# Optimization experiments

Measured on AMD Instinct MI355X. Metric: run time of the kernel, lower is better.

## Reference

```python
import jax, jax.numpy as jnp
import numpy as np

N0, N1, N2 = 30000, 90000, 60000          # nodes, edges, triangles
D_IN, D_OUT, HEADS = 256, 128, 4
NNZ0, NNZ1, NNZ2 = 960000, 180000, 180000  # sparse incidence nnz


def setup_inputs() -> dict:
    key = jax.random.key(0)
    ks = jax.random.split(key, 18)
    s = 0.05
    return {
        "x0": jax.random.normal(ks[0], (N0, D_IN), dtype=jnp.float32),
        "x1": jax.random.normal(ks[1], (N1, D_IN), dtype=jnp.float32),
        "x2": jax.random.normal(ks[2], (N2, D_IN), dtype=jnp.float32),
        "rows0": jax.random.randint(ks[3], (NNZ0,), 0, N0),
        "cols0": jax.random.randint(ks[4], (NNZ0,), 0, N0),
        "rows1": jax.random.randint(ks[5], (NNZ1,), 0, N0),
        "cols1": jax.random.randint(ks[6], (NNZ1,), 0, N1),
        "rows2": jax.random.randint(ks[7], (NNZ2,), 0, N0),
        "cols2": jax.random.randint(ks[8], (NNZ2,), 0, N2),
        # per-head parameters (SATLayer_regular), stacked on leading head axis
        "W1": jax.random.normal(ks[9], (HEADS, D_IN, D_OUT), dtype=jnp.float32) * s,
        "b1": jax.random.normal(ks[10], (HEADS, D_OUT), dtype=jnp.float32) * s,
        "a1_w": jax.random.normal(ks[11], (HEADS, D_OUT), dtype=jnp.float32) * s,
        "a1_b": jax.random.normal(ks[12], (HEADS,), dtype=jnp.float32) * s,
        "a2_w": jax.random.normal(ks[13], (HEADS, D_OUT), dtype=jnp.float32) * s,
        "a2_b": jax.random.normal(ks[14], (HEADS,), dtype=jnp.float32) * s,
        "Wagg": jax.random.normal(ks[15], (HEADS, 4 * D_OUT, D_OUT), dtype=jnp.float32) * s,
        "bagg": jax.random.normal(ks[16], (HEADS, D_OUT), dtype=jnp.float32) * s,
    }


def reference(x0, x1, x2, rows0, cols0, rows1, cols1, rows2, cols2,
              W1, b1, a1_w, a1_b, a2_w, a2_b, Wagg, bagg):
    n0 = x0.shape[0]

    def sat_head(W1h, b1h, a1wh, a1bh, a2wh, a2bh, Waggh, baggh):
        # shared Linearlayer1 + ReLU applied to all simplex levels
        xi0 = jax.nn.relu(x0 @ W1h + b1h)   # [n0, d]
        xj1 = jax.nn.relu(x1 @ W1h + b1h)   # [n1, d]
        xj2 = jax.nn.relu(x2 @ W1h + b1h)   # [n2, d]
        a1 = xi0 @ a1wh + a1bh              # [n0] attention source term

        def attention_agg(xj, rows, cols):
            a2 = xj @ a2wh + a2bh                              # [nj]
            att = jax.nn.sigmoid(a1[rows] + a2[cols])          # [nnz]
            msg = att[:, None] * xj[cols]                      # [nnz, d]
            return jax.ops.segment_sum(msg, rows, num_segments=n0)

        agg0 = attention_agg(xi0, rows0, cols0)
        agg1 = attention_agg(xj1, rows1, cols1)
        agg2 = attention_agg(xj2, rows2, cols2)
        cat = jnp.concatenate([xi0, agg0, agg1, agg2], axis=1)  # [n0, 4d]
        return cat @ Waggh + baggh                              # [n0, d]

    # stack over heads, then mean (layer0_1 + torch.mean)
    outs = jax.vmap(sat_head)(W1, b1, a1_w, a1_b, a2_w, a2_b, Wagg, bagg)
    return jnp.mean(outs, axis=0)
```

## Files before the change

### kernel.cpp

```cpp
#include <hip/hip_runtime.h>

typedef __attribute__((ext_vector_type(8))) short short8;
typedef __attribute__((ext_vector_type(4))) float f32x4;
typedef unsigned short ushort_t;
typedef unsigned int uint32;

#define N0 30000
#define N1 90000
#define N2 60000
#define P0 30208
#define P1 90112
#define P2 60032
#define S1OFF 30208
#define S2OFF 120320
#define MPAD 180352
#define MT_ALL 1409
#define MT0 236
#define MT1 704
#define MT2 469
#define NNZ_ALL 1320000

__device__ __forceinline__ float bf2f(ushort_t u) {
    union { uint32 i; float f; } v; v.i = ((uint32)u) << 16; return v.f;
}
__device__ __forceinline__ ushort_t f2bf(float f) {
    union { float f; uint32 i; } v; v.f = f;
    uint32 x = v.i;
    x += ((x >> 16) & 1u) + 0x7FFFu;
    return (ushort_t)(x >> 16);
}

__global__ __launch_bounds__(256) void prep_w(const float* __restrict__ W1,
                                              const float* __restrict__ Wagg,
                                              const float* __restrict__ bagg,
                                              ushort_t* __restrict__ W1t,
                                              ushort_t* __restrict__ Wgt,
                                              ushort_t* __restrict__ WgtC,
                                              float* __restrict__ bsum) {
    int idx = blockIdx.x * blockDim.x + threadIdx.x;
    if (idx < 131072) {
        int h = idx >> 15, rem = idx & 32767, n = rem >> 8, k = rem & 255;
        W1t[idx] = f2bf(W1[((size_t)h * 256 + k) * 128 + n]);
    }
    if (idx < 196608) {
        int h = idx / 49152, rem = idx % 49152;
        int l = rem / 16384, rem2 = rem % 16384, n = rem2 >> 7, k = rem2 & 127;
        Wgt[idx] = f2bf(Wagg[((size_t)h * 512 + (l + 1) * 128 + k) * 128 + n]);
    }
    if (idx < 65536) {
        int n = idx >> 9, kk = idx & 511, h = kk >> 7, k = kk & 127;
        WgtC[idx] = f2bf(Wagg[((size_t)h * 512 + k) * 128 + n]);
    }
    if (idx < 128) {
        float s = 0.f;
        #pragma unroll
        for (int h = 0; h < 4; ++h) s += bagg[h * 128 + idx];
        bsum[idx] = s;
    }
}

__global__ __launch_bounds__(256) void csr_zero(int* __restrict__ cur) {
    int i = blockIdx.x * blockDim.x + threadIdx.x;
    if (i < P0) cur[i] = 0;
}

__global__ __launch_bounds__(256) void csr_hist(const int* __restrict__ rows, int nE,
                                                int* __restrict__ cur) {
    int i = blockIdx.x * blockDim.x + threadIdx.x;
    if (i < nE) atomicAdd(cur + rows[i], 1);
}

__global__ __launch_bounds__(1024) void csr_scan(int* __restrict__ cur,
                                                 int* __restrict__ rowPtr) {
    __shared__ int ssum[1024];
    const int t = threadIdx.x;
    const int base = t * 30;
    int loc[30];
    int s = 0;
    #pragma unroll
    for (int i = 0; i < 30; ++i) {
        int r = base + i;
        int v = (r < N0) ? cur[r] : 0;
        loc[i] = s; s += v;
    }
    ssum[t] = s;
    __syncthreads();
    for (int off = 1; off < 1024; off <<= 1) {
        int v = (t >= off) ? ssum[t - off] : 0;
        __syncthreads();
        ssum[t] += v;
        __syncthreads();
    }
    int carry = (t == 0) ? 0 : ssum[t - 1];
    #pragma unroll
    for (int i = 0; i < 30; ++i) {
        int r = base + i;
        if (r < N0) {
            int p = carry + loc[i];
            rowPtr[r] = p;
            cur[r] = p;
        }
    }
    if (t == 0) rowPtr[N0] = NNZ_ALL;
}

__global__ __launch_bounds__(256) void csr_scatter(const int* __restrict__ rows,
                                                   const int* __restrict__ cols,
                                                   int nE, int Sl,
                                                   int* __restrict__ cur,
                                                   int* __restrict__ sortedCg) {
    int i = blockIdx.x * blockDim.x + threadIdx.x;
    if (i < nE) {
        int pos = atomicAdd(cur + rows[i], 1);
        sortedCg[pos] = Sl + cols[i];
    }
}

__global__ __launch_bounds__(256) void gemm_x(const float* __restrict__ x0,
                                              const float* __restrict__ x1,
                                              const float* __restrict__ x2,
                                              const ushort_t* __restrict__ W1t,
                                              const float* __restrict__ b1,
                                              ushort_t* __restrict__ Y) {
    __shared__ ushort_t As[128 * 264];
    __shared__ ushort_t Bs[128 * 40];
    const int tid = threadIdx.x;
    const int lane = tid & 63;
    const int wid = tid >> 6;
    const int wm = wid >> 1, wn = wid & 1;
    const int l15 = lane & 15, lg = lane >> 4;
    const int r0 = blockIdx.x * 128;

    const float* src; int jbase, nreal;
    if (r0 < P0)          { src = x0; jbase = r0;         nreal = N0; }
    else if (r0 < S2OFF)  { src = x1; jbase = r0 - S1OFF; nreal = N1; }
    else                  { src = x2; jbase = r0 - S2OFF; nreal = N2; }

    for (int c = 0; c < 32; ++c) {
        int f = tid + c * 256;
        int row = f >> 6, col4 = f & 63;
        int j = jbase + row;
        float vx = 0.f, vy = 0.f, vz = 0.f, vw = 0.f;
        if (j < nreal) {
            const float4 v = *(const float4*)(src + (size_t)j * 256 + col4 * 4);
            vx = v.x; vy = v.y; vz = v.z; vw = v.w;
        }
        ushort_t o[4] __attribute__((aligned(8)));
        o[0] = f2bf(vx); o[1] = f2bf(vy); o[2] = f2bf(vz); o[3] = f2bf(vw);
        *(uint2*)(As + row * 264 + col4 * 4) = *(const uint2*)o;
    }
    __syncthreads();

    for (int h = 0; h < 4; ++h) {
        f32x4 acc[4][4] = {};
        const ushort_t* Bh = W1t + h * 32768;
        for (int kt = 0; kt < 256; kt += 32) {
            #pragma unroll
            for (int u = 0; u < 2; ++u) {
                int g = tid * 2 + u;
                int n = g >> 2, kc = g & 3;
                *(uint4*)(Bs + n * 40 + kc * 8) = *(const uint4*)(Bh + n * 256 + kt + kc * 8);
            }
            __syncthreads();
            short8 af[4], bfr[4];
            #pragma unroll
            for (int m = 0; m < 4; ++m)
                af[m] = *(const short8*)(As + (wm * 64 + m * 16 + l15) * 264 + kt + lg * 8);
            #pragma unroll
            for (int n = 0; n < 4; ++n)
                bfr[n] = *(const short8*)(Bs + (wn * 64 + n * 16 + l15) * 40 + lg * 8);
            #pragma unroll
            for (int m = 0; m < 4; ++m)
                #pragma unroll
                for (int n = 0; n < 4; ++n)
                    acc[m][n] = __builtin_amdgcn_mfma_f32_16x16x32_bf16(af[m], bfr[n], acc[m][n], 0, 0, 0);
            __syncthreads();
        }
        #pragma unroll
        for (int n = 0; n < 4; ++n) {
            int col = wn * 64 + n * 16 + l15;
            float bb = b1[h * 128 + col];
            #pragma unroll
            for (int m = 0; m < 4; ++m)
            #pragma unroll
            for (int j = 0; j < 4; ++j) {
                int row = r0 + wm * 64 + m * 16 + lg * 4 + j;
                float v = acc[m][n][j] + bb;
                v = v > 0.f ? v : 0.f;
                Y[(size_t)row * 512 + h * 128 + col] = f2bf(v);
            }
        }
    }
}

template<int EPI>
__global__ __launch_bounds__(256)
void gemm_k(const ushort_t* A, int ldA, int strideA,
            const ushort_t* __restrict__ B, int K, int strideB,
            ushort_t* outBF, int outLd, int strideOut,
            float* __restrict__ outF,
            const float* __restrict__ bias, int strideBias,
            int rowGuard)
{
    __shared__ ushort_t As[128 * 40];
    __shared__ ushort_t Bs[128 * 40];
    const int tid = threadIdx.x;
    const int lane = tid & 63;
    const int wid = tid >> 6;
    const int wm = wid >> 1, wn = wid & 1;
    const int r0 = blockIdx.x * 128;
    const int l15 = lane & 15, lg = lane >> 4;

    A += (size_t)blockIdx.y * strideA;
    B += (size_t)blockIdx.y * strideB;
    if (outBF) outBF += (size_t)blockIdx.y * strideOut;
    if (bias) bias += (size_t)blockIdx.y * strideBias;

    f32x4 acc[4][4] = {};

    for (int kt = 0; kt < K; kt += 32) {
        #pragma unroll
        for (int c = 0; c < 2; ++c) {
            int idx = tid + c * 256;
            int row = idx >> 2, kc = idx & 3;
            uint4 va = *(const uint4*)(A + (size_t)(r0 + row) * ldA + kt + kc * 8);
            *(uint4*)(As + row * 40 + kc * 8) = va;
            uint4 vb = *(const uint4*)(B + (size_t)row * K + kt + kc * 8);
            *(uint4*)(Bs + row * 40 + kc * 8) = vb;
        }
        __syncthreads();
        short8 af[4], bfr[4];
        #pragma unroll
        for (int m = 0; m < 4; ++m)
            af[m] = *(const short8*)(As + (wm * 64 + m * 16 + l15) * 40 + lg * 8);
        #pragma unroll
        for (int n = 0; n < 4; ++n)
            bfr[n] = *(const short8*)(Bs + (wn * 64 + n * 16 + l15) * 40 + lg * 8);
        #pragma unroll
        for (int m = 0; m < 4; ++m)
            #pragma unroll
            for (int n = 0; n < 4; ++n)
                acc[m][n] = __builtin_amdgcn_mfma_f32_16x16x32_bf16(af[m], bfr[n], acc[m][n], 0, 0, 0);
        __syncthreads();
    }

    #pragma unroll
    for (int m = 0; m < 4; ++m)
    #pragma unroll
    for (int n = 0; n < 4; ++n)
    #pragma unroll
    for (int j = 0; j < 4; ++j) {
        int row = r0 + wm * 64 + m * 16 + lg * 4 + j;
        int col = wn * 64 + n * 16 + l15;
        float v = acc[m][n][j];
        if (EPI == 1) {
            outBF[(size_t)row * outLd + col] = f2bf(v);
        } else {
            if (row < rowGuard) outF[(size_t)row * 128 + col] = 0.25f * (v + bias[col]);
        }
    }
}

__global__ __launch_bounds__(256) void attn_coef(const ushort_t* __restrict__ Y,
                                                 const float* __restrict__ a1w,
                                                 const float* __restrict__ a1b,
                                                 const float* __restrict__ a2w,
                                                 const float* __restrict__ a2b,
                                                 float* __restrict__ a1o,
                                                 float* __restrict__ a2o) {
    int tid = threadIdx.x, lane = tid & 63, wid = tid >> 6;
    int R = blockIdx.x * 4 + wid;
    int h = lane >> 4, s = lane & 15;
    uint4 v = *(const uint4*)(Y + (size_t)R * 512 + h * 128 + s * 8);
    const ushort_t* u = (const ushort_t*)&v;
    float x[8];
    #pragma unroll
    for (int i = 0; i < 8; ++i) x[i] = bf2f(u[i]);
    float d2 = 0.f;
    #pragma unroll
    for (int i = 0; i < 8; ++i) d2 += x[i] * a2w[h * 128 + s * 8 + i];
    #pragma unroll
    for (int off = 1; off < 16; off <<= 1) d2 += __shfl_xor(d2, off);
    if (s == 0) a2o[(size_t)h * MPAD + R] = d2 + a2b[h];
    if (R < N0) {
        float d1 = 0.f;
        #pragma unroll
        for (int i = 0; i < 8; ++i) d1 += x[i] * a1w[h * 128 + s * 8 + i];
        #pragma unroll
        for (int off = 1; off < 16; off <<= 1) d1 += __shfl_xor(d1, off);
        if (s == 0) a1o[(size_t)h * P0 + R] = d1 + a1b[h];
    }
}

__global__ __launch_bounds__(256) void pull_agg(const int* __restrict__ rowPtr,
                                                const int* __restrict__ sortedCg,
                                                const float* __restrict__ a1,
                                                const float* __restrict__ a2,
                                                const ushort_t* __restrict__ z,
                                                float* __restrict__ out) {
    int w = blockIdx.x * 4 + (threadIdx.x >> 6);
    if (w >= N0) return;
    const int lane = threadIdx.x & 63;
    const int h = lane >> 4, g = lane & 15;

    const float a1r = a1[(size_t)h * P0 + w];
    const float* a2h = a2 + (size_t)h * MPAD;
    int beg = rowPtr[w], end = rowPtr[w + 1];

    float acc[8] = {0.f, 0.f, 0.f, 0.f, 0.f, 0.f, 0.f, 0.f};
    for (int e = beg; e < end; ++e) {
        int cg = sortedCg[e];
        float s = a1r + a2h[cg];
        float att = 0.25f / (1.f + __expf(-s));
        uint4 v = *(const uint4*)(z + (size_t)cg * 512 + lane * 8);
        const ushort_t* u = (const ushort_t*)&v;
        #pragma unroll
        for (int j = 0; j < 8; ++j) acc[j] += att * bf2f(u[j]);
    }
    #pragma unroll
    for (int j = 0; j < 8; ++j) {
        acc[j] += __shfl_xor(acc[j], 16);
        acc[j] += __shfl_xor(acc[j], 32);
    }
    float2* p = (float2*)(out + (size_t)w * 128 + g * 8 + h * 2);
    float2 o = *p;
    o.x += acc[h * 2 + 0];
    o.y += acc[h * 2 + 1];
    *p = o;
}

extern "C" void kernel_launch(void* const* d_in, const int* in_sizes, int n_in,
                              void* d_out, int out_size, void* d_ws, size_t ws_size,
                              hipStream_t stream) {
    const float* x0   = (const float*)d_in[0];
    const float* x1   = (const float*)d_in[1];
    const float* x2   = (const float*)d_in[2];
    const int* rows0  = (const int*)d_in[3];
    const int* cols0  = (const int*)d_in[4];
    const int* rows1  = (const int*)d_in[5];
    const int* cols1  = (const int*)d_in[6];
    const int* rows2  = (const int*)d_in[7];
    const int* cols2  = (const int*)d_in[8];
    const float* W1   = (const float*)d_in[9];
    const float* b1   = (const float*)d_in[10];
    const float* a1w  = (const float*)d_in[11];
    const float* a1b  = (const float*)d_in[12];
    const float* a2w  = (const float*)d_in[13];
    const float* a2b  = (const float*)d_in[14];
    const float* Wagg = (const float*)d_in[15];
    const float* bagg = (const float*)d_in[16];
    float* out = (float*)d_out;
    char* ws = (char*)d_ws;

    ushort_t* Y      = (ushort_t*)(ws);
    float*    a1o    = (float*)(ws + 184680448);
    float*    a2o    = (float*)(ws + 185163776);
    ushort_t* W1t    = (ushort_t*)(ws + 188049408);
    ushort_t* Wgt    = (ushort_t*)(ws + 188311552);
    ushort_t* WgtC   = (ushort_t*)(ws + 188704768);
    float*    bsum   = (float*)(ws + 188835840);
    int*      cur    = (int*)(ws + 188836352);
    int*      rowPtr = (int*)(ws + 188957184);
    int*      srtCg  = (int*)(ws + 189078016);

    csr_zero<<<(P0 + 255) / 256, 256, 0, stream>>>(cur);
    csr_hist<<<(960000 + 255) / 256, 256, 0, stream>>>(rows0, 960000, cur);
    csr_hist<<<(180000 + 255) / 256, 256, 0, stream>>>(rows1, 180000, cur);
    csr_hist<<<(180000 + 255) / 256, 256, 0, stream>>>(rows2, 180000, cur);
    csr_scan<<<1, 1024, 0, stream>>>(cur, rowPtr);
    csr_scatter<<<(960000 + 255) / 256, 256, 0, stream>>>(rows0, cols0, 960000, 0, cur, srtCg);
    csr_scatter<<<(180000 + 255) / 256, 256, 0, stream>>>(rows1, cols1, 180000, S1OFF, cur, srtCg);
    csr_scatter<<<(180000 + 255) / 256, 256, 0, stream>>>(rows2, cols2, 180000, S2OFF, cur, srtCg);

    prep_w<<<768, 256, 0, stream>>>(W1, Wagg, bagg, W1t, Wgt, WgtC, bsum);
    gemm_x<<<MT_ALL, 256, 0, stream>>>(x0, x1, x2, W1t, b1, Y);

    attn_coef<<<MPAD / 4, 256, 0, stream>>>(Y, a1w, a1b, a2w, a2b, a1o, a2o);

    gemm_k<2><<<dim3(MT0, 1), 256, 0, stream>>>(
        Y, 512, 0, WgtC, 512, 0, nullptr, 0, 0, out, bsum, 0, N0);

    gemm_k<1><<<dim3(MT0, 4), 256, 0, stream>>>(
        Y, 512, 128, Wgt + 0 * 16384, 128, 3 * 16384, Y, 512, 128, nullptr, nullptr, 0, 0);
    gemm_k<1><<<dim3(MT1, 4), 256, 0, stream>>>(
        Y + (size_t)S1OFF * 512, 512, 128, Wgt + 1 * 16384, 128, 3 * 16384,
        Y + (size_t)S1OFF * 512, 512, 128, nullptr, nullptr, 0, 0);
    gemm_k<1><<<dim3(MT2, 4), 256, 0, stream>>>(
        Y + (size_t)S2OFF * 512, 512, 128, Wgt + 2 * 16384, 128, 3 * 16384,
        Y + (size_t)S2OFF * 512, 512, 128, nullptr, nullptr, 0, 0);

    pull_agg<<<(N0 + 3) / 4, 256, 0, stream>>>(rowPtr, srtCg, a1o, a2o, Y, out);
}
```

Baseline: 699.3 us.

## Fuse attention coefficients into per-level Z GEMM and split CSR per level

Folds the attention-coefficient dot products into a single merged GEMM that projects each head's activations by the level-specific aggregation weights. The full 128x128 tile and K=128 are staged in LDS once, removing the separate attn_coef pass and its extra read of Y. The CSR build is split into three per-level structures with three pull_agg launches, and the pull loop is unrolled by two edges. The three launches add traffic on the output accumulator, and the fused kernel uses far more shared memory per block, which may reduce occupancy.

Measured after the change: 645.1 us. -7.7%, faster.

```diff
diff --git a/kernel.cpp b/kernel.cpp
--- a/kernel.cpp
+++ b/kernel.cpp
@@ -9,16 +9,15 @@
 #define N1 90000
 #define N2 60000
 #define P0 30208
-#define P1 90112
-#define P2 60032
 #define S1OFF 30208
 #define S2OFF 120320
 #define MPAD 180352
 #define MT_ALL 1409
 #define MT0 236
-#define MT1 704
-#define MT2 469
-#define NNZ_ALL 1320000
+#define NE0 960000
+#define NE1 180000
+#define NE2 180000
+#define CSTRIDE 30720
 
 __device__ __forceinline__ float bf2f(ushort_t u) {
     union { uint32 i; float f; } v; v.i = ((uint32)u) << 16; return v.f;
@@ -61,7 +60,7 @@
 
 __global__ __launch_bounds__(256) void csr_zero(int* __restrict__ cur) {
     int i = blockIdx.x * blockDim.x + threadIdx.x;
-    if (i < P0) cur[i] = 0;
+    if (i < 3 * CSTRIDE) cur[i] = 0;
 }
 
 __global__ __launch_bounds__(256) void csr_hist(const int* __restrict__ rows, int nE,
@@ -70,9 +69,14 @@
     if (i < nE) atomicAdd(cur + rows[i], 1);
 }
 
-__global__ __launch_bounds__(1024) void csr_scan(int* __restrict__ cur,
-                                                 int* __restrict__ rowPtr) {
+__global__ __launch_bounds__(1024) void csr_scan(int* __restrict__ curA,
+                                                 int* __restrict__ rowPtrA,
+                                                 int nE0, int nE1, int nE2) {
     __shared__ int ssum[1024];
+    const int b = blockIdx.x;
+    int* cur = curA + b * CSTRIDE;
+    int* rowPtr = rowPtrA + b * CSTRIDE;
+    const int nE = (b == 0) ? nE0 : (b == 1 ? nE1 : nE2);
     const int t = threadIdx.x;
     const int base = t * 30;
     int loc[30];
@@ -101,7 +105,7 @@
             cur[r] = p;
         }
     }
-    if (t == 0) rowPtr[N0] = NNZ_ALL;
+    if (t == 0) rowPtr[N0] = nE;
 }
 
 __global__ __launch_bounds__(256) void csr_scatter(const int* __restrict__ rows,
@@ -193,14 +197,11 @@
     }
 }
 
-template<int EPI>
 __global__ __launch_bounds__(256)
-void gemm_k(const ushort_t* A, int ldA, int strideA,
-            const ushort_t* __restrict__ B, int K, int strideB,
-            ushort_t* outBF, int outLd, int strideOut,
-            float* __restrict__ outF,
-            const float* __restrict__ bias, int strideBias,
-            int rowGuard)
+void gemm_init(const ushort_t* __restrict__ A,
+               const ushort_t* __restrict__ B,
+               float* __restrict__ outF,
+               const float* __restrict__ bias)
 {
     __shared__ ushort_t As[128 * 40];
     __shared__ ushort_t Bs[128 * 40];
@@ -211,21 +212,16 @@
     const int r0 = blockIdx.x * 128;
     const int l15 = lane & 15, lg = lane >> 4;
 
-    A += (size_t)blockIdx.y * strideA;
-    B += (size_t)blockIdx.y * strideB;
-    if (outBF) outBF += (size_t)blockIdx.y * strideOut;
-    if (bias) bias += (size_t)blockIdx.y * strideBias;
-
     f32x4 acc[4][4] = {};
 
-    for (int kt = 0; kt < K; kt += 32) {
+    for (int kt = 0; kt < 512; kt += 32) {
         #pragma unroll
         for (int c = 0; c < 2; ++c) {
             int idx = tid + c * 256;
             int row = idx >> 2, kc = idx & 3;
-            uint4 va = *(const uint4*)(A + (size_t)(r0 + row) * ldA + kt + kc * 8);
+            uint4 va = *(const uint4*)(A + (size_t)(r0 + row) * 512 + kt + kc * 8);
             *(uint4*)(As + row * 40 + kc * 8) = va;
-            uint4 vb = *(const uint4*)(B + (size_t)row * K + kt + kc * 8);
+            uint4 vb = *(const uint4*)(B + (size_t)row * 512 + kt + kc * 8);
             *(uint4*)(Bs + row * 40 + kc * 8) = vb;
         }
         __syncthreads();
@@ -252,43 +248,95 @@
     for (int j = 0; j < 4; ++j) {
         int row = r0 + wm * 64 + m * 16 + lg * 4 + j;
         int col = wn * 64 + n * 16 + l15;
-        float v = acc[m][n][j];
-        if (EPI == 1) {
-            outBF[(size_t)row * outLd + col] = f2bf(v);
-        } else {
-            if (row < rowGuard) outF[(size_t)row * 128 + col] = 0.25f * (v + bias[col]);
-        }
-    }
-}
-
-__global__ __launch_bounds__(256) void attn_coef(const ushort_t* __restrict__ Y,
-                                                 const float* __restrict__ a1w,
-                                                 const float* __restrict__ a1b,
-                                                 const float* __restrict__ a2w,
-                                                 const float* __restrict__ a2b,
-                                                 float* __restrict__ a1o,
-                                                 float* __restrict__ a2o) {
-    int tid = threadIdx.x, lane = tid & 63, wid = tid >> 6;
-    int R = blockIdx.x * 4 + wid;
-    int h = lane >> 4, s = lane & 15;
-    uint4 v = *(const uint4*)(Y + (size_t)R * 512 + h * 128 + s * 8);
-    const ushort_t* u = (const ushort_t*)&v;
-    float x[8];
-    #pragma unroll
-    for (int i = 0; i < 8; ++i) x[i] = bf2f(u[i]);
-    float d2 = 0.f;
-    #pragma unroll
-    for (int i = 0; i < 8; ++i) d2 += x[i] * a2w[h * 128 + s * 8 + i];
-    #pragma unroll
-    for (int off = 1; off < 16; off <<= 1) d2 += __shfl_xor(d2, off);
-    if (s == 0) a2o[(size_t)h * MPAD + R] = d2 + a2b[h];
-    if (R < N0) {
-        float d1 = 0.f;
-        #pragma unroll
-        for (int i = 0; i < 8; ++i) d1 += x[i] * a1w[h * 128 + s * 8 + i];
-        #pragma unroll
-        for (int off = 1; off < 16; off <<= 1) d1 += __shfl_xor(d1, off);
-        if (s == 0) a1o[(size_t)h * P0 + R] = d1 + a1b[h];
+        if (row < N0) outF[(size_t)row * 128 + col] = 0.25f * (acc[m][n][j] + bias[col]);
+    }
+}
+
+__global__ __launch_bounds__(256) void gemm_z(const ushort_t* Yin,
+                                              const ushort_t* __restrict__ Wgt,
+                                              const float* __restrict__ a1w,
+                                              const float* __restrict__ a1b,
+                                              const float* __restrict__ a2w,
+                                              const float* __restrict__ a2b,
+                                              float* __restrict__ a1o,
+                                              float* __restrict__ a2o,
+                                              ushort_t* Yout) {
+    __shared__ ushort_t As[128 * 136];
+    __shared__ ushort_t Bs[128 * 136];
+    __shared__ float a1wS[128], a2wS[128];
+    const int tid = threadIdx.x;
+    const int h = blockIdx.y;
+    const int r0 = blockIdx.x * 128;
+    const int l = (r0 < P0) ? 0 : (r0 < S2OFF ? 1 : 2);
+    const ushort_t* B = Wgt + ((h * 3 + l) << 14);
+
+    if (tid < 128) {
+        a1wS[tid] = a1w[h * 128 + tid];
+        a2wS[tid] = a2w[h * 128 + tid];
+    }
+    #pragma unroll
+    for (int c = 0; c < 8; ++c) {
+        int idx = tid + c * 256;
+        int row = idx >> 4, ch = idx & 15;
+        *(uint4*)(As + row * 136 + ch * 8) =
+            *(const uint4*)(Yin + (size_t)(r0 + row) * 512 + h * 128 + ch * 8);
+        *(uint4*)(Bs + row * 136 + ch * 8) = *(const uint4*)(B + row * 128 + ch * 8);
+    }
+    __syncthreads();
+
+    {
+        int row = tid >> 1, half = tid & 1;
+        const ushort_t* yr = As + row * 136 + half * 64;
+        float d1 = 0.f, d2 = 0.f;
+        #pragma unroll
+        for (int t = 0; t < 8; ++t) {
+            short8 v = *(const short8*)(yr + t * 8);
+            #pragma unroll
+            for (int j = 0; j < 8; ++j) {
+                float f = bf2f(((const ushort_t*)&v)[j]);
+                d2 += f * a2wS[half * 64 + t * 8 + j];
+                d1 += f * a1wS[half * 64 + t * 8 + j];
+            }
+        }
+        d2 += __shfl_xor(d2, 1);
+        d1 += __shfl_xor(d1, 1);
+        if (half == 0) {
+            a2o[(size_t)h * MPAD + r0 + row] = d2 + a2b[h];
+            if (l == 0) a1o[(size_t)h * P0 + r0 + row] = d1 + a1b[h];
+        }
+    }
+
+    const int lane = tid & 63;
+    const int wid = tid >> 6;
+    const int wm = wid >> 1, wn = wid & 1;
+    const int l15 = lane & 15, lg = lane >> 4;
+
+    f32x4 acc[4][4] = {};
+    #pragma unroll
+    for (int kt = 0; kt < 128; kt += 32) {
+        short8 af[4], bfr[4];
+        #pragma unroll
+        for (int m = 0; m < 4; ++m)
+            af[m] = *(const short8*)(As + (wm * 64 + m * 16 + l15) * 136 + kt + lg * 8);
+        #pragma unroll
+        for (int n = 0; n < 4; ++n)
+            bfr[n] = *(const short8*)(Bs + (wn * 64 + n * 16 + l15) * 136 + kt + lg * 8);
+        #pragma unroll
+        for (int m = 0; m < 4; ++m)
+            #pragma unroll
+            for (int n = 0; n < 4; ++n)
+                acc[m][n] = __builtin_amdgcn_mfma_f32_16x16x32_bf16(af[m], bfr[n], acc[m][n], 0, 0, 0);
+    }
+
+    #pragma unroll
+    for (int m = 0; m < 4; ++m)
+    #pragma unroll
+    for (int n = 0; n < 4; ++n)
+    #pragma unroll
+    for (int j = 0; j < 4; ++j) {
+        int row = r0 + wm * 64 + m * 16 + lg * 4 + j;
+        int col = wn * 64 + n * 16 + l15;
+        Yout[(size_t)row * 512 + h * 128 + col] = f2bf(acc[m][n][j]);
     }
 }
 
@@ -308,7 +356,22 @@
     int beg = rowPtr[w], end = rowPtr[w + 1];
 
     float acc[8] = {0.f, 0.f, 0.f, 0.f, 0.f, 0.f, 0.f, 0.f};
-    for (int e = beg; e < end; ++e) {
+    int e = beg;
+    for (; e + 1 < end; e += 2) {
+        int cg0 = sortedCg[e], cg1 = sortedCg[e + 1];
+        float s0 = a1r + a2h[cg0];
+        float s1 = a1r + a2h[cg1];
+        float att0 = 0.25f / (1.f + __expf(-s0));
+        float att1 = 0.25f / (1.f + __expf(-s1));
+        uint4 v0 = *(const uint4*)(z + (size_t)cg0 * 512 + lane * 8);
+        uint4 v1 = *(const uint4*)(z + (size_t)cg1 * 512 + lane * 8);
+        const ushort_t* u0 = (const ushort_t*)&v0;
+        const ushort_t* u1 = (const ushort_t*)&v1;
+        #pragma unroll
+        for (int j = 0; j < 8; ++j)
+            acc[j] += att0 * bf2f(u0[j]) + att1 * bf2f(u1[j]);
+    }
+    if (e < end) {
         int cg = sortedCg[e];
         float s = a1r + a2h[cg];
         float att = 0.25f / (1.f + __expf(-s));
@@ -360,34 +423,30 @@
     ushort_t* WgtC   = (ushort_t*)(ws + 188704768);
     float*    bsum   = (float*)(ws + 188835840);
     int*      cur    = (int*)(ws + 188836352);
-    int*      rowPtr = (int*)(ws + 188957184);
-    int*      srtCg  = (int*)(ws + 189078016);
-
-    csr_zero<<<(P0 + 255) / 256, 256, 0, stream>>>(cur);
-    csr_hist<<<(960000 + 255) / 256, 256, 0, stream>>>(rows0, 960000, cur);
-    csr_hist<<<(180000 + 255) / 256, 256, 0, stream>>>(rows1, 180000, cur);
-    csr_hist<<<(180000 + 255) / 256, 256, 0, stream>>>(rows2, 180000, cur);
-    csr_scan<<<1, 1024, 0, stream>>>(cur, rowPtr);
-    csr_scatter<<<(960000 + 255) / 256, 256, 0, stream>>>(rows0, cols0, 960000, 0, cur, srtCg);
-    csr_scatter<<<(180000 + 255) / 256, 256, 0, stream>>>(rows1, cols1, 180000, S1OFF, cur, srtCg);
-    csr_scatter<<<(180000 + 255) / 256, 256, 0, stream>>>(rows2, cols2, 180000, S2OFF, cur, srtCg);
+    int*      rowPtr = (int*)(ws + 189204992);
+    int*      srtCg  = (int*)(ws + 189573632);
+
+    int* cur0 = cur,              * cur1 = cur + CSTRIDE,    * cur2 = cur + 2 * CSTRIDE;
+    int* rp0  = rowPtr,           * rp1  = rowPtr + CSTRIDE, * rp2  = rowPtr + 2 * CSTRIDE;
+    int* srt0 = srtCg,            * srt1 = srtCg + NE0,      * srt2 = srtCg + NE0 + NE1;
+
+    csr_zero<<<(3 * CSTRIDE + 255) / 256, 256, 0, stream>>>(cur);
+    csr_hist<<<(NE0 + 255) / 256, 256, 0, stream>>>(rows0, NE0, cur0);
+    csr_hist<<<(NE1 + 255) / 256, 256, 0, stream>>>(rows1, NE1, cur1);
+    csr_hist<<<(NE2 + 255) / 256, 256, 0, stream>>>(rows2, NE2, cur2);
+    csr_scan<<<3, 1024, 0, stream>>>(cur, rowPtr, NE0, NE1, NE2);
+    csr_scatter<<<(NE0 + 255) / 256, 256, 0, stream>>>(rows0, cols0, NE0, 0,     cur0, srt0);
+    csr_scatter<<<(NE1 + 255) / 256, 256, 0, stream>>>(rows1, cols1, NE1, S1OFF, cur1, srt1);
+    csr_scatter<<<(NE2 + 255) / 256, 256, 0, stream>>>(rows2, cols2, NE2, S2OFF, cur2, srt2);
 
     prep_w<<<768, 256, 0, stream>>>(W1, Wagg, bagg, W1t, Wgt, WgtC, bsum);
     gemm_x<<<MT_ALL, 256, 0, stream>>>(x0, x1, x2, W1t, b1, Y);
 
-    attn_coef<<<MPAD / 4, 256, 0, stream>>>(Y, a1w, a1b, a2w, a2b, a1o, a2o);
-
-    gemm_k<2><<<dim3(MT0, 1), 256, 0, stream>>>(
-        Y, 512, 0, WgtC, 512, 0, nullptr, 0, 0, out, bsum, 0, N0);
-
-    gemm_k<1><<<dim3(MT0, 4), 256, 0, stream>>>(
-        Y, 512, 128, Wgt + 0 * 16384, 128, 3 * 16384, Y, 512, 128, nullptr, nullptr, 0, 0);
-    gemm_k<1><<<dim3(MT1, 4), 256, 0, stream>>>(
-        Y + (size_t)S1OFF * 512, 512, 128, Wgt + 1 * 16384, 128, 3 * 16384,
-        Y + (size_t)S1OFF * 512, 512, 128, nullptr, nullptr, 0, 0);
-    gemm_k<1><<<dim3(MT2, 4), 256, 0, stream>>>(
-        Y + (size_t)S2OFF * 512, 512, 128, Wgt + 2 * 16384, 128, 3 * 16384,
-        Y + (size_t)S2OFF * 512, 512, 128, nullptr, nullptr, 0, 0);
-
-    pull_agg<<<(N0 + 3) / 4, 256, 0, stream>>>(rowPtr, srtCg, a1o, a2o, Y, out);
-}
+    gemm_init<<<MT0, 256, 0, stream>>>(Y, WgtC, out, bsum);
+
+    gemm_z<<<dim3(MT_ALL, 4), 256, 0, stream>>>(Y, Wgt, a1w, a1b, a2w, a2b, a1o, a2o, Y);
+
+    pull_agg<<<(N0 + 3) / 4, 256, 0, stream>>>(rp0, srt0, a1o, a2o, Y, out);
+    pull_agg<<<(N0 + 3) / 4, 256, 0, stream>>>(rp1, srt1, a1o, a2o, Y, out);
+    pull_agg<<<(N0 + 3) / 4, 256, 0, stream>>>(rp2, srt2, a1o, a2o, Y, out);
+}
```
